# Kernel tuning notes

Measured on AMD Instinct MI355X. Metric: run time of the kernel, lower is better.

The kernel has to match this reference:

```python
import jax, jax.numpy as jnp
import numpy as np

N_NODES = 50000
N_EDGES = 10000
NNZ = 1600000
IN_DIM = 256
OUT_DIM = 128


def setup_inputs() -> dict:
    key = jax.random.key(0)
    k1, k2, k3, k4, k5 = jax.random.split(key, 5)
    X = jax.random.normal(k1, (N_NODES, IN_DIM), dtype=jnp.float32)
    theta = jax.random.normal(k2, (IN_DIM, OUT_DIM), dtype=jnp.float32) * (1.0 / np.sqrt(IN_DIM))
    bias = jax.random.normal(k3, (OUT_DIM,), dtype=jnp.float32) * 0.01
    node_idx = jax.random.randint(k4, (NNZ,), 0, N_NODES, dtype=jnp.int32)
    hyedge_idx = jax.random.randint(k5, (NNZ,), 0, N_EDGES, dtype=jnp.int32)
    return {
        "X": X,
        "theta": theta,
        "bias": bias,
        "node_idx": node_idx,
        "hyedge_idx": hyedge_idx,
        "num_nodes": N_NODES,
        "num_edges": N_EDGES,
    }


def reference(X, theta, bias, node_idx, hyedge_idx, num_nodes, num_edges):
    # Dense transform: [N, in] @ [in, out] -> [N, out]
    Xt = X @ theta
    # MA_v: vertex -> hyperedge aggregation (gather by node_idx, scatter_add by hyedge_idx)
    Y = jax.ops.segment_sum(Xt[node_idx], hyedge_idx, num_segments=num_edges)  # [M, out]
    # MA_e: hyperedge -> vertex aggregation (gather by hyedge_idx, scatter_add by node_idx)
    X_new = jax.ops.segment_sum(Y[hyedge_idx], node_idx, num_segments=num_nodes)  # [N, out]
    # U_v: bias add
    return X_new + bias
```

## Files before the change

kernel.cpp:

```cpp
#include <hip/hip_runtime.h>
#include <hip/hip_bf16.h>

#define NN 50000
#define NE 10000
#define KD 256
#define MD 128

#define NCAP 76

#define RNG 4
#define RDIV 12500
#define ERCAP 96

#define NB_E 313
#define NB_N 196
#define NBT  (NB_E + NB_N)
#define CCAP_E 5760
#define CCAP_N 8960

#define NCB 256
#define GEMM_TILES ((NN + 255) / 256)
#define CPB 6272
#define RPT ((CPB + 511) / 512)

#define AGG_BLKS ((NE + 7) / 8 * RNG)

typedef __attribute__((ext_vector_type(8))) short short8;
typedef __attribute__((ext_vector_type(4))) float f32x4;

union ABfrag { short8 s; unsigned u[4]; };

__device__ inline unsigned pack_bf2(float a, float b) {
    __hip_bfloat162 h = __float22bfloat162_rn(make_float2(a, b));
    return *reinterpret_cast<unsigned*>(&h);
}

__device__ inline unsigned short bf16_1(float a) {
    __hip_bfloat16 h = __float2bfloat16(a);
    return *reinterpret_cast<unsigned short*>(&h);
}

__device__ inline float bf_lo(unsigned v) { return __uint_as_float(v << 16); }
__device__ inline float bf_hi(unsigned v) { return __uint_as_float(v & 0xffff0000u); }

__device__ inline void exscan_block(const int* __restrict__ cnt, int* __restrict__ lst,
                                    int n, int* buf, int tid) {
    int v = (tid < n) ? cnt[tid] : 0;
    buf[tid] = v;
    __syncthreads();
    #pragma unroll
    for (int s = 1; s < 512; s <<= 1) {
        int t = (tid >= s) ? buf[tid - s] : 0;
        __syncthreads();
        buf[tid] += t;
        __syncthreads();
    }
    if (tid < n) lst[tid] = buf[tid] - v;
    __syncthreads();
}

__global__ __launch_bounds__(256) void prep_theta(const float* __restrict__ Th,
                                                  unsigned short* __restrict__ tT,
                                                  int* __restrict__ ccur) {
    int tid = threadIdx.x;
    if (blockIdx.x == 0) { ccur[tid] = 0; ccur[tid + 256] = 0; }
    int gid = blockIdx.x * 256 + tid;
    int k = gid >> 7, c = gid & 127;
    tT[(size_t)c * KD + k] = bf16_1(Th[(size_t)k * MD + c]);
}

__global__ __launch_bounds__(512) void coarse_gemm(const float* __restrict__ X,
                                                   const unsigned short* __restrict__ tT,
                                                   unsigned short* __restrict__ XtU, int N,
                                                   const int* __restrict__ nidx,
                                                   const int* __restrict__ eidx,
                                                   int* __restrict__ ccur,
                                                   unsigned* __restrict__ coarse_e,
                                                   unsigned* __restrict__ coarse_n, int nnz) {
    __shared__ unsigned srt[CPB];
    __shared__ int cnt[NBT], lst[NBT], gb[NBT];
    __shared__ int wsum[8], wpre[8];
    const int tid = threadIdx.x;
    const int wv = tid >> 6, lane = tid & 63;

    {
        const int cbid = blockIdx.x;
        int C = (nnz + NCB - 1) / NCB;
        if (C > CPB) C = CPB;
        const int k0 = cbid * C;
        int k1 = k0 + C; if (k1 > nnz) k1 = nnz;
        const int nk = k1 - k0;

        for (int j = tid; j < NBT; j += 512) cnt[j] = 0;
        __syncthreads();

        unsigned rr[RPT];
        #pragma unroll
        for (int it = 0; it < RPT; ++it) {
            int i = tid + it * 512;
            unsigned r = 0u;
            if (i < nk) {
                int e = eidx[k0 + i], n = nidx[k0 + i];
                r = ((unsigned)n << 14) | (unsigned)e;
                atomicAdd(&cnt[e >> 5], 1);
                atomicAdd(&cnt[NB_E + (n >> 8)], 1);
            }
            rr[it] = r;
        }
        __syncthreads();

        {
            int myv = (tid < NBT) ? cnt[tid] : 0;
            int v = myv;
            #pragma unroll
            for (int s = 1; s < 64; s <<= 1) {
                int t = __shfl_up(v, s);
                if (lane >= s) v += t;
            }
            if (lane == 63) wsum[wv] = v;
            __syncthreads();
            if (wv == 0) {
                int u = (lane < 8) ? wsum[lane] : 0;
                #pragma unroll
                for (int s = 1; s < 8; s <<= 1) {
                    int t = __shfl_up(u, s);
                    if (lane >= s) u += t;
                }
                if (lane < 8) wpre[lane] = u - wsum[lane];
            }
            __syncthreads();
            if (tid < NBT) lst[tid] = v - myv + wpre[wv];
            __syncthreads();
        }

        for (int j = tid; j < NBT; j += 512) {
            int c = cnt[j];
            gb[j] = c ? atomicAdd(&ccur[j], c) : 0;
            cnt[j] = 0;
        }
        __syncthreads();

        #pragma unroll
        for (int it = 0; it < RPT; ++it) {
            int i = tid + it * 512;
            if (i < nk) {
                unsigned r = rr[it];
                int b = (r & 0x3FFF) >> 5;
                int rk = atomicAdd(&cnt[b], 1);
                srt[lst[b] + rk] = r;
            }
        }
        __syncthreads();
        for (int p = tid; p < nk; p += 512) {
            unsigned r = srt[p];
            int b = (r & 0x3FFF) >> 5;
            int g = gb[b] + (p - lst[b]);
            if (g < CCAP_E) coarse_e[(size_t)b * CCAP_E + g] = r;
        }
        __syncthreads();

        #pragma unroll
        for (int it = 0; it < RPT; ++it) {
            int i = tid + it * 512;
            if (i < nk) {
                unsigned r = rr[it];
                int b = NB_E + ((int)(r >> 14) >> 8);
                int rk = atomicAdd(&cnt[b], 1);
                srt[(lst[b] - nk) + rk] = r;
            }
        }
        __syncthreads();
        for (int p = tid; p < nk; p += 512) {
            unsigned r = srt[p];
            int b = NB_E + ((int)(r >> 14) >> 8);
            int g = gb[b] + (p - (lst[b] - nk));
            if (g < CCAP_N) coarse_n[(size_t)(b - NB_E) * CCAP_N + g] = r;
        }
    }

    if (blockIdx.x < GEMM_TILES) {
        const int lr = lane & 15;
        const int lk = lane >> 4;
        const int row0 = blockIdx.x * 256 + wv * 32;
        const int rowA = row0 + lr;
        const int rowB = row0 + 16 + lr;

        f32x4 acc0[8], acc1[8];
        #pragma unroll
        for (int ct = 0; ct < 8; ++ct) {
            acc0[ct] = (f32x4){0.f, 0.f, 0.f, 0.f};
            acc1[ct] = (f32x4){0.f, 0.f, 0.f, 0.f};
        }

        const short8* tTv = (const short8*)tT;
        #pragma unroll
        for (int ks = 0; ks < 8; ++ks) {
            ABfrag a0, a1;
            if (rowA < N) {
                const float* xp = X + (size_t)rowA * KD + ks * 32 + lk * 8;
                float4 v0 = *(const float4*)(xp);
                float4 v1 = *(const float4*)(xp + 4);
                a0.u[0] = pack_bf2(v0.x, v0.y);
                a0.u[1] = pack_bf2(v0.z, v0.w);
                a0.u[2] = pack_bf2(v1.x, v1.y);
                a0.u[3] = pack_bf2(v1.z, v1.w);
            } else a0.u[0] = a0.u[1] = a0.u[2] = a0.u[3] = 0u;
            if (rowB < N) {
                const float* xp = X + (size_t)rowB * KD + ks * 32 + lk * 8;
                float4 v0 = *(const float4*)(xp);
                float4 v1 = *(const float4*)(xp + 4);
                a1.u[0] = pack_bf2(v0.x, v0.y);
                a1.u[1] = pack_bf2(v0.z, v0.w);
                a1.u[2] = pack_bf2(v1.x, v1.y);
                a1.u[3] = pack_bf2(v1.z, v1.w);
            } else a1.u[0] = a1.u[1] = a1.u[2] = a1.u[3] = 0u;

            #pragma unroll
            for (int ct = 0; ct < 8; ++ct) {
                ABfrag b;
                b.s = tTv[(size_t)(ct * 16 + lr) * 32 + ks * 4 + lk];
                acc0[ct] = __builtin_amdgcn_mfma_f32_16x16x32_bf16(a0.s, b.s, acc0[ct], 0, 0, 0);
                acc1[ct] = __builtin_amdgcn_mfma_f32_16x16x32_bf16(a1.s, b.s, acc1[ct], 0, 0, 0);
            }
        }

        #pragma unroll
        for (int ct = 0; ct < 8; ++ct) {
            #pragma unroll
            for (int i = 0; i < 4; ++i) {
                int rA = row0 + lk * 4 + i;
                int rB = row0 + 16 + lk * 4 + i;
                if (rA < N) XtU[(size_t)rA * MD + ct * 16 + lr] = bf16_1(acc0[ct][i]);
                if (rB < N) XtU[(size_t)rB * MD + ct * 16 + lr] = bf16_1(acc1[ct][i]);
            }
        }
    }
}

__global__ __launch_bounds__(512) void fine_e(const unsigned* __restrict__ coarse_e,
                                              const int* __restrict__ ccur,
                                              unsigned short* __restrict__ e_slots,
                                              int* __restrict__ e_cnt) {
    __shared__ unsigned srt[CCAP_E];
    __shared__ int cnt[128], lst[128];
    const int tid = threadIdx.x;
    const int b = blockIdx.x;

    const unsigned* buf = coarse_e + (size_t)b * CCAP_E;
    int m = ccur[b]; if (m > CCAP_E) m = CCAP_E;

    for (int j = tid; j < 128; j += 512) cnt[j] = 0;
    __syncthreads();
    for (int i = tid; i < m; i += 512) {
        unsigned r = buf[i];
        int e = r & 0x3FFF;
        int n = (int)(r >> 14);
        atomicAdd(&cnt[((e & 31) << 2) | (n / RDIV)], 1);
    }
    __syncthreads();
    exscan_block(cnt, lst, 128, (int*)srt, tid);
    if (tid < 128) {
        int e = b * 32 + (tid >> 2);
        if (e < NE) {
            int c = cnt[tid]; if (c > ERCAP) c = ERCAP;
            e_cnt[e * RNG + (tid & 3)] = c;
        }
    }
    __syncthreads();
    for (int j = tid; j < 128; j += 512) cnt[j] = 0;
    __syncthreads();
    for (int i = tid; i < m; i += 512) {
        unsigned r = buf[i];
        int e = r & 0x3FFF;
        unsigned n = r >> 14;
        int li = ((e & 31) << 2) | ((int)n / RDIV);
        int rk = atomicAdd(&cnt[li], 1);
        srt[lst[li] + rk] = ((unsigned)li << 16) | n;
    }
    __syncthreads();
    for (int p = tid; p < m; p += 512) {
        unsigned v = srt[p];
        int li = (int)(v >> 16);
        int lr = p - lst[li];
        if (lr < ERCAP) {
            int e = b * 32 + (li >> 2);
            e_slots[((size_t)e * RNG + (li & 3)) * ERCAP + lr] = (unsigned short)(v & 0xFFFF);
        }
    }
}

__global__ __launch_bounds__(512) void fine_n_agg_ve(const unsigned* __restrict__ coarse_n,
                                                     const int* __restrict__ ccur,
                                                     unsigned short* __restrict__ n_slots,
                                                     int* __restrict__ n_cnt,
                                                     const unsigned* __restrict__ XtB,
                                                     const int* __restrict__ e_cnt,
                                                     const unsigned short* __restrict__ e_slots,
                                                     unsigned* __restrict__ P) {
    __shared__ unsigned srt[CCAP_N];
    __shared__ int cnt[256], lst[256];
    const int tid = threadIdx.x;

    if (blockIdx.x < NB_N) {
        const int bb = blockIdx.x;
        const unsigned* buf = coarse_n + (size_t)bb * CCAP_N;
        int m = ccur[NB_E + bb]; if (m > CCAP_N) m = CCAP_N;

        for (int j = tid; j < 256; j += 512) cnt[j] = 0;
        __syncthreads();
        for (int i = tid; i < m; i += 512) {
            unsigned r = buf[i];
            atomicAdd(&cnt[(r >> 14) & 255], 1);
        }
        __syncthreads();
        exscan_block(cnt, lst, 256, (int*)srt, tid);
        if (tid < 256) {
            int g = bb * 256 + tid;
            if (g < NN) {
                int c = cnt[tid]; if (c > NCAP) c = NCAP;
                n_cnt[g] = c;
            }
        }
        __syncthreads();
        for (int j = tid; j < 256; j += 512) cnt[j] = 0;
        __syncthreads();
        for (int i = tid; i < m; i += 512) {
            unsigned r = buf[i];
            int k = (r >> 14) & 255;
            int rk = atomicAdd(&cnt[k], 1);
            srt[lst[k] + rk] = ((unsigned)k << 16) | (r & 0x3FFF);
        }
        __syncthreads();
        for (int p = tid; p < m; p += 512) {
            unsigned v = srt[p];
            int k = (int)(v >> 16);
            int lr = p - lst[k];
            if (lr < NCAP) {
                int g = bb * 256 + k;
                n_slots[(size_t)g * NCAP + lr] = (unsigned short)(v & 0x3FFF);
            }
        }
        return;
    }

    const int wid = blockIdx.x - NB_N;
    const int r = wid & 3;
    const int g = wid >> 2;
    int wave = g * 8 + (tid >> 6);
    int l    = tid & 63;
    const int grp = l >> 3, sub = l & 7;
    int ec = e_cnt[wave * RNG + r]; if (ec > ERCAP) ec = ERCAP;
    const unsigned short* slots = e_slots + ((size_t)wave * RNG + r) * ERCAP;
    const uint4* Xv = (const uint4*)XtB;

    float a[16];
    #pragma unroll
    for (int i = 0; i < 16; ++i) a[i] = 0.f;

    for (int c = 0; c < ec; c += 64) {
        int m = ec - c; if (m > 64) m = 64;
        int idx = (c + l < ec) ? (int)slots[c + l] : 0;
        for (int j = 0; j < m; j += 8) {
            int mem = j + grp;
            bool valid = mem < m;
            int n = __shfl(idx, valid ? mem : 0);
            const uint4* row = Xv + (size_t)n * 16 + sub * 2;
            uint4 v0 = row[0];
            uint4 v1 = row[1];
            if (valid) {
                a[0]  += bf_lo(v0.x); a[1]  += bf_hi(v0.x);
                a[2]  += bf_lo(v0.y); a[3]  += bf_hi(v0.y);
                a[4]  += bf_lo(v0.z); a[5]  += bf_hi(v0.z);
                a[6]  += bf_lo(v0.w); a[7]  += bf_hi(v0.w);
                a[8]  += bf_lo(v1.x); a[9]  += bf_hi(v1.x);
                a[10] += bf_lo(v1.y); a[11] += bf_hi(v1.y);
                a[12] += bf_lo(v1.z); a[13] += bf_hi(v1.z);
                a[14] += bf_lo(v1.w); a[15] += bf_hi(v1.w);
            }
        }
    }
    #pragma unroll
    for (int i = 0; i < 16; ++i) {
        a[i] += __shfl_xor(a[i], 8);
        a[i] += __shfl_xor(a[i], 16);
        a[i] += __shfl_xor(a[i], 32);
    }
    if (l < 8) {
        uint4 o0 = make_uint4(pack_bf2(a[0],  a[1]),  pack_bf2(a[2],  a[3]),
                              pack_bf2(a[4],  a[5]),  pack_bf2(a[6],  a[7]));
        uint4 o1 = make_uint4(pack_bf2(a[8],  a[9]),  pack_bf2(a[10], a[11]),
                              pack_bf2(a[12], a[13]), pack_bf2(a[14], a[15]));
        uint4* prow = (uint4*)P + ((size_t)r * NE + wave) * 16 + sub * 2;
        prow[0] = o0;
        prow[1] = o1;
    }
}

__global__ __launch_bounds__(256) void reduce_y(const unsigned* __restrict__ P,
                                                unsigned* __restrict__ YB) {
    int gid = blockIdx.x * 256 + threadIdx.x;
    if (gid >= NE * 64) return;
    float a = 0.f, b = 0.f;
    #pragma unroll
    for (int r = 0; r < RNG; ++r) {
        unsigned v = P[(size_t)r * NE * 64 + gid];
        a += bf_lo(v);
        b += bf_hi(v);
    }
    YB[gid] = pack_bf2(a, b);
}

__global__ __launch_bounds__(256) void agg_ev(const unsigned* __restrict__ YB,
                                              const int* __restrict__ n_cnt,
                                              const unsigned short* __restrict__ n_slots,
                                              const float* __restrict__ bias,
                                              float* __restrict__ out) {
    int wave = blockIdx.x * 4 + (threadIdx.x >> 6);
    int l    = threadIdx.x & 63;
    if (wave >= NN) return;
    const int grp = l >> 3, sub = l & 7;
    int cnt = n_cnt[wave]; if (cnt > NCAP) cnt = NCAP;
    const unsigned short* slots = n_slots + (size_t)wave * NCAP;
    const uint4* Yv = (const uint4*)YB;

    float a[16];
    #pragma unroll
    for (int i = 0; i < 16; ++i) a[i] = 0.f;

    for (int c = 0; c < cnt; c += 64) {
        int m = cnt - c; if (m > 64) m = 64;
        int idx = (c + l < cnt) ? (int)slots[c + l] : 0;
        for (int j = 0; j < m; j += 8) {
            int mem = j + grp;
            bool valid = mem < m;
            int e = __shfl(idx, valid ? mem : 0);
            const uint4* row = Yv + (size_t)e * 16 + sub * 2;
            uint4 v0 = row[0];
            uint4 v1 = row[1];
            if (valid) {
                a[0]  += bf_lo(v0.x); a[1]  += bf_hi(v0.x);
                a[2]  += bf_lo(v0.y); a[3]  += bf_hi(v0.y);
                a[4]  += bf_lo(v0.z); a[5]  += bf_hi(v0.z);
                a[6]  += bf_lo(v0.w); a[7]  += bf_hi(v0.w);
                a[8]  += bf_lo(v1.x); a[9]  += bf_hi(v1.x);
                a[10] += bf_lo(v1.y); a[11] += bf_hi(v1.y);
                a[12] += bf_lo(v1.z); a[13] += bf_hi(v1.z);
                a[14] += bf_lo(v1.w); a[15] += bf_hi(v1.w);
            }
        }
    }
    #pragma unroll
    for (int i = 0; i < 16; ++i) {
        a[i] += __shfl_xor(a[i], 8);
        a[i] += __shfl_xor(a[i], 16);
        a[i] += __shfl_xor(a[i], 32);
    }
    if (l < 8) {
        float4* orow = (float4*)(out + (size_t)wave * MD);
        #pragma unroll
        for (int q = 0; q < 4; ++q) {
            float4 bq = ((const float4*)bias)[sub * 4 + q];
            float4 o = make_float4(a[q * 4 + 0] + bq.x, a[q * 4 + 1] + bq.y,
                                   a[q * 4 + 2] + bq.z, a[q * 4 + 3] + bq.w);
            orow[sub * 4 + q] = o;
        }
    }
}

extern "C" void kernel_launch(void* const* d_in, const int* in_sizes, int n_in,
                              void* d_out, int out_size, void* d_ws, size_t ws_size,
                              hipStream_t stream) {
    const float* X     = (const float*)d_in[0];
    const float* theta = (const float*)d_in[1];
    const float* bias  = (const float*)d_in[2];
    const int*   nidx  = (const int*)d_in[3];
    const int*   eidx  = (const int*)d_in[4];
    float*       out   = (float*)d_out;

    const int N   = in_sizes[0] / KD;
    const int nnz = in_sizes[3];

    char* w = (char*)d_ws;
    unsigned*       XtB      = (unsigned*)w;       w += (size_t)NN * MD * 2;
    unsigned*       YB       = (unsigned*)w;       w += (size_t)NE * MD * 2;
    int*            e_cnt    = (int*)w;            w += (size_t)NE * RNG * 4;
    int*            n_cnt    = (int*)w;            w += (size_t)NN * 4;
    int*            ccur     = (int*)w;            w += (size_t)512 * 4;
    unsigned short* thetaT   = (unsigned short*)w; w += (size_t)MD * KD * 2;
    unsigned*       P        = (unsigned*)w;       w += (size_t)RNG * NE * 64 * 4;
    unsigned*       coarse_e = (unsigned*)w;       w += (size_t)NB_E * CCAP_E * 4;
    unsigned*       coarse_n = (unsigned*)w;       w += (size_t)NB_N * CCAP_N * 4;
    unsigned short* e_slots  = (unsigned short*)w; w += (size_t)NE * RNG * ERCAP * 2;
    unsigned short* n_slots  = (unsigned short*)w;

    prep_theta<<<(MD * KD) / 256, 256, 0, stream>>>(theta, thetaT, ccur);

    coarse_gemm<<<NCB, 512, 0, stream>>>(X, thetaT, (unsigned short*)XtB, N,
                                         nidx, eidx, ccur,
                                         coarse_e, coarse_n, nnz);

    fine_e<<<NB_E, 512, 0, stream>>>(coarse_e, ccur, e_slots, e_cnt);

    fine_n_agg_ve<<<NB_N + AGG_BLKS, 512, 0, stream>>>(coarse_n, ccur, n_slots, n_cnt,
                                                       XtB, e_cnt, e_slots, P);

    reduce_y<<<(NE * 64 + 255) / 256, 256, 0, stream>>>(P, YB);

    agg_ev<<<(NN + 3) / 4, 256, 0, stream>>>(YB, n_cnt, n_slots, bias, out);
}
```

Measured before the change: 133.3 us.

## Split coarse binning and GEMM into separate blocks of one launch, vectorise index loads

The fused kernel used to have every block do a binning chunk and then a GEMM tile in sequence. Now it launches 256 binning blocks plus 196 separate GEMM blocks, so the two kinds of work run concurrently on different CUs instead of serially inside one block. The binning path also reads the edge and node indices as int4 vectors with a fixed span of 6252 per block. This assumes nnz is a multiple of 4 and that each chunk start is 16-byte aligned, which holds because 6252 is divisible by 4. The cost is more blocks and register pressure from holding 16 entries per thread.

```diff
diff --git a/kernel.cpp b/kernel.cpp
--- a/kernel.cpp
+++ b/kernel.cpp
@@ -18,12 +18,11 @@
 #define CCAP_E 5760
 #define CCAP_N 8960
 
+#define GEMM_BLKS ((NN + 255) / 256)
 #define NCB 256
-#define GEMM_TILES ((NN + 255) / 256)
+#define CSPAN 6252
 #define CPB 6272
-#define RPT ((CPB + 511) / 512)
-
-#define AGG_BLKS ((NE + 7) / 8 * RNG)
+#define VIT 4
 
 typedef __attribute__((ext_vector_type(8))) short short8;
 typedef __attribute__((ext_vector_type(4))) float f32x4;
@@ -69,7 +68,7 @@
     tT[(size_t)c * KD + k] = bf16_1(Th[(size_t)k * MD + c]);
 }
 
-__global__ __launch_bounds__(512) void coarse_gemm(const float* __restrict__ X,
+__global__ __launch_bounds__(512) void gemm_coarse(const float* __restrict__ X,
                                                    const unsigned short* __restrict__ tT,
                                                    unsigned short* __restrict__ XtU, int N,
                                                    const int* __restrict__ nidx,
@@ -83,105 +82,10 @@
     const int tid = threadIdx.x;
     const int wv = tid >> 6, lane = tid & 63;
 
-    {
-        const int cbid = blockIdx.x;
-        int C = (nnz + NCB - 1) / NCB;
-        if (C > CPB) C = CPB;
-        const int k0 = cbid * C;
-        int k1 = k0 + C; if (k1 > nnz) k1 = nnz;
-        const int nk = k1 - k0;
-
-        for (int j = tid; j < NBT; j += 512) cnt[j] = 0;
-        __syncthreads();
-
-        unsigned rr[RPT];
-        #pragma unroll
-        for (int it = 0; it < RPT; ++it) {
-            int i = tid + it * 512;
-            unsigned r = 0u;
-            if (i < nk) {
-                int e = eidx[k0 + i], n = nidx[k0 + i];
-                r = ((unsigned)n << 14) | (unsigned)e;
-                atomicAdd(&cnt[e >> 5], 1);
-                atomicAdd(&cnt[NB_E + (n >> 8)], 1);
-            }
-            rr[it] = r;
-        }
-        __syncthreads();
-
-        {
-            int myv = (tid < NBT) ? cnt[tid] : 0;
-            int v = myv;
-            #pragma unroll
-            for (int s = 1; s < 64; s <<= 1) {
-                int t = __shfl_up(v, s);
-                if (lane >= s) v += t;
-            }
-            if (lane == 63) wsum[wv] = v;
-            __syncthreads();
-            if (wv == 0) {
-                int u = (lane < 8) ? wsum[lane] : 0;
-                #pragma unroll
-                for (int s = 1; s < 8; s <<= 1) {
-                    int t = __shfl_up(u, s);
-                    if (lane >= s) u += t;
-                }
-                if (lane < 8) wpre[lane] = u - wsum[lane];
-            }
-            __syncthreads();
-            if (tid < NBT) lst[tid] = v - myv + wpre[wv];
-            __syncthreads();
-        }
-
-        for (int j = tid; j < NBT; j += 512) {
-            int c = cnt[j];
-            gb[j] = c ? atomicAdd(&ccur[j], c) : 0;
-            cnt[j] = 0;
-        }
-        __syncthreads();
-
-        #pragma unroll
-        for (int it = 0; it < RPT; ++it) {
-            int i = tid + it * 512;
-            if (i < nk) {
-                unsigned r = rr[it];
-                int b = (r & 0x3FFF) >> 5;
-                int rk = atomicAdd(&cnt[b], 1);
-                srt[lst[b] + rk] = r;
-            }
-        }
-        __syncthreads();
-        for (int p = tid; p < nk; p += 512) {
-            unsigned r = srt[p];
-            int b = (r & 0x3FFF) >> 5;
-            int g = gb[b] + (p - lst[b]);
-            if (g < CCAP_E) coarse_e[(size_t)b * CCAP_E + g] = r;
-        }
-        __syncthreads();
-
-        #pragma unroll
-        for (int it = 0; it < RPT; ++it) {
-            int i = tid + it * 512;
-            if (i < nk) {
-                unsigned r = rr[it];
-                int b = NB_E + ((int)(r >> 14) >> 8);
-                int rk = atomicAdd(&cnt[b], 1);
-                srt[(lst[b] - nk) + rk] = r;
-            }
-        }
-        __syncthreads();
-        for (int p = tid; p < nk; p += 512) {
-            unsigned r = srt[p];
-            int b = NB_E + ((int)(r >> 14) >> 8);
-            int g = gb[b] + (p - (lst[b] - nk));
-            if (g < CCAP_N) coarse_n[(size_t)(b - NB_E) * CCAP_N + g] = r;
-        }
-    }
-
-    if (blockIdx.x < GEMM_TILES) {
+    if (blockIdx.x >= NCB) {
         const int lr = lane & 15;
         const int lk = lane >> 4;
-        const int row0 = blockIdx.x * 256 + wv * 32;
+        const int row0 = (blockIdx.x - NCB) * 256 + wv * 32;
         const int rowA = row0 + lr;
         const int rowB = row0 + 16 + lr;
 
@@ -234,6 +138,112 @@
                 if (rB < N) XtU[(size_t)rB * MD + ct * 16 + lr] = bf16_1(acc1[ct][i]);
             }
         }
+        return;
+    }
+
+    const int k0 = blockIdx.x * CSPAN;
+    int k1 = k0 + CSPAN; if (k1 > nnz) k1 = nnz;
+    const int nk = (k1 > k0) ? (k1 - k0) : 0;
+
+    for (int j = tid; j < NBT; j += 512) cnt[j] = 0;
+    __syncthreads();
+
+    const int4* e4 = (const int4*)(eidx + k0);
+    const int4* n4 = (const int4*)(nidx + k0);
+    unsigned rr[VIT * 4];
+    #pragma unroll
+    for (int it = 0; it < VIT; ++it) {
+        int vi = tid + it * 512;
+        int base = vi * 4;
+        int4 ev = make_int4(0, 0, 0, 0), nv = make_int4(0, 0, 0, 0);
+        if (base < nk) { ev = e4[vi]; nv = n4[vi]; }
+        #pragma unroll
+        for (int j = 0; j < 4; ++j) {
+            int e = (j == 0) ? ev.x : (j == 1) ? ev.y : (j == 2) ? ev.z : ev.w;
+            int n = (j == 0) ? nv.x : (j == 1) ? nv.y : (j == 2) ? nv.z : nv.w;
+            unsigned r = 0u;
+            if (base + j < nk) {
+                r = ((unsigned)n << 14) | (unsigned)e;
+                atomicAdd(&cnt[e >> 5], 1);
+                atomicAdd(&cnt[NB_E + (n >> 8)], 1);
+            }
+            rr[it * 4 + j] = r;
+        }
+    }
+    __syncthreads();
+
+    {
+        int myv = (tid < NBT) ? cnt[tid] : 0;
+        int v = myv;
+        #pragma unroll
+        for (int s = 1; s < 64; s <<= 1) {
+            int t = __shfl_up(v, s);
+            if (lane >= s) v += t;
+        }
+        if (lane == 63) wsum[wv] = v;
+        __syncthreads();
+        if (wv == 0) {
+            int u = (lane < 8) ? wsum[lane] : 0;
+            #pragma unroll
+            for (int s = 1; s < 8; s <<= 1) {
+                int t = __shfl_up(u, s);
+                if (lane >= s) u += t;
+            }
+            if (lane < 8) wpre[lane] = u - wsum[lane];
+        }
+        __syncthreads();
+        if (tid < NBT) lst[tid] = v - myv + wpre[wv];
+        __syncthreads();
+    }
+
+    for (int j = tid; j < NBT; j += 512) {
+        int c = cnt[j];
+        gb[j] = c ? atomicAdd(&ccur[j], c) : 0;
+        cnt[j] = 0;
+    }
+    __syncthreads();
+
+    #pragma unroll
+    for (int it = 0; it < VIT; ++it) {
+        #pragma unroll
+        for (int j = 0; j < 4; ++j) {
+            int i = (tid + it * 512) * 4 + j;
+            if (i < nk) {
+                unsigned r = rr[it * 4 + j];
+                int b = (r & 0x3FFF) >> 5;
+                int rk = atomicAdd(&cnt[b], 1);
+                srt[lst[b] + rk] = r;
+            }
+        }
+    }
+    __syncthreads();
+    for (int p = tid; p < nk; p += 512) {
+        unsigned r = srt[p];
+        int b = (r & 0x3FFF) >> 5;
+        int g = gb[b] + (p - lst[b]);
+        if (g < CCAP_E) coarse_e[(size_t)b * CCAP_E + g] = r;
+    }
+    __syncthreads();
+
+    #pragma unroll
+    for (int it = 0; it < VIT; ++it) {
+        #pragma unroll
+        for (int j = 0; j < 4; ++j) {
+            int i = (tid + it * 512) * 4 + j;
+            if (i < nk) {
+                unsigned r = rr[it * 4 + j];
+                int b = NB_E + ((int)(r >> 14) >> 8);
+                int rk = atomicAdd(&cnt[b], 1);
+                srt[(lst[b] - nk) + rk] = r;
+            }
+        }
+    }
+    __syncthreads();
+    for (int p = tid; p < nk; p += 512) {
+        unsigned r = srt[p];
+        int b = NB_E + ((int)(r >> 14) >> 8);
+        int g = gb[b] + (p - (lst[b] - nk));
+        if (g < CCAP_N) coarse_n[(size_t)(b - NB_E) * CCAP_N + g] = r;
     }
 }
 
@@ -288,6 +298,8 @@
         }
     }
 }
+
+#define AGG_BLKS ((NE + 7) / 8 * RNG)
 
 __global__ __launch_bounds__(512) void fine_n_agg_ve(const unsigned* __restrict__ coarse_n,
                                                      const int* __restrict__ ccur,
@@ -495,9 +507,9 @@
 
     prep_theta<<<(MD * KD) / 256, 256, 0, stream>>>(theta, thetaT, ccur);
 
-    coarse_gemm<<<NCB, 512, 0, stream>>>(X, thetaT, (unsigned short*)XtB, N,
-                                         nidx, eidx, ccur,
-                                         coarse_e, coarse_n, nnz);
+    gemm_coarse<<<NCB + GEMM_BLKS, 512, 0, stream>>>(X, thetaT, (unsigned short*)XtB, N,
+                                                     nidx, eidx, ccur,
+                                                     coarse_e, coarse_n, nnz);
 
     fine_e<<<NB_E, 512, 0, stream>>>(coarse_e, ccur, e_slots, e_cnt);
 
```

After: 125.2 us. 6.1% less time.
